# Optimization experiments

Measured on AMD Instinct MI355X. Metric: run time of the kernel, lower is better.

Reference implementation:

```python
import jax, jax.numpy as jnp
import numpy as np

Q_SIZE = 1024
K_SIZE = 1024
NUM_UNITS = 1024
B, T_Q, T_K = 16, 64, 128


def setup_inputs() -> dict:
    key = jax.random.key(0)
    k1, k2, k3, k4, k5 = jax.random.split(key, 5)
    stdv = 1.0 / np.sqrt(NUM_UNITS)
    query = jax.random.normal(k1, (B, T_Q, Q_SIZE), dtype=jnp.float32)
    keys = jax.random.normal(k2, (B, T_K, K_SIZE), dtype=jnp.float32)
    # nn.Linear(in, out, bias=False) weight has shape (out, in)
    Wq = jax.random.uniform(k3, (NUM_UNITS, Q_SIZE), dtype=jnp.float32,
                            minval=-stdv, maxval=stdv)
    Wk = jax.random.uniform(k4, (NUM_UNITS, K_SIZE), dtype=jnp.float32,
                            minval=-stdv, maxval=stdv)
    linear_att = jax.random.uniform(k5, (NUM_UNITS,), dtype=jnp.float32,
                                    minval=-stdv, maxval=stdv)
    normalize_scalar = jnp.full((1,), stdv, dtype=jnp.float32)
    normalize_bias = jnp.zeros((NUM_UNITS,), dtype=jnp.float32)
    return {"query": query, "keys": keys, "Wq": Wq, "Wk": Wk,
            "linear_att": linear_att, "normalize_scalar": normalize_scalar,
            "normalize_bias": normalize_bias}


def reference(query, keys, Wq, Wk, linear_att, normalize_scalar, normalize_bias):
    # batch_first=True, 3-d query, math='fp32', normalize=True, dropout=0, no mask
    att_query = jnp.einsum('bqi,ni->bqn', query, Wq)   # (b, t_q, n)
    att_keys = jnp.einsum('bki,ni->bkn', keys, Wk)     # (b, t_k, n)
    # broadcast sum + bias: (b, t_q, t_k, n)
    sum_qk = att_query[:, :, None, :] + att_keys[:, None, :, :] + normalize_bias
    la = linear_att / jnp.linalg.norm(linear_att)
    la = la * normalize_scalar  # (n,) via broadcast with (1,)
    scores = jnp.einsum('bqkn,n->bqk', jnp.tanh(sum_qk), la)  # (b, t_q, t_k)
    scores_normalized = jax.nn.softmax(scores, axis=-1)
    context = jnp.einsum('bqk,bkn->bqn', scores_normalized, keys)
    return context, scores_normalized
```

## Files before the change

### kernel.cpp

```cpp
#include <hip/hip_runtime.h>
#include <hip/hip_bf16.h>
#include <math.h>


#define ALPHA_2LOG2E 2.8853900817779268f
#define LOG2E 1.4426950408889634f

typedef __attribute__((ext_vector_type(8))) short short8;
typedef __attribute__((ext_vector_type(4))) float f32x4;
typedef __attribute__((ext_vector_type(2))) float f32x2;

static __device__ __forceinline__ short f2bf(float f) {
    union { float f; unsigned u; } v; v.f = f;
    unsigned r = v.u + 0x7fffu + ((v.u >> 16) & 1u);
    return (short)(r >> 16);
}

static __device__ __forceinline__ void gload16(const void* g, void* l) {
    __builtin_amdgcn_global_load_lds(
        (const __attribute__((address_space(1))) unsigned*)g,
        (__attribute__((address_space(3))) unsigned*)l, 16, 0, 0);
}

__global__ __launch_bounds__(256) void cast_prep_kernel(
    const float* __restrict__ q, const float* __restrict__ k,
    const float* __restrict__ wq, const float* __restrict__ wk,
    short* __restrict__ qb, short* __restrict__ kb,
    short* __restrict__ wqb, short* __restrict__ wkb,
    const float* __restrict__ la, const float* __restrict__ scal,
    float* __restrict__ la2, float* __restrict__ sla)
{
    const int bid = blockIdx.x;
    if (bid == 2560) {
        __shared__ float red[4];
        const int t = threadIdx.x, lane = t & 63, w = t >> 6;
        float ss = 0.f;
        for (int i = t; i < 1024; i += 256) { float v = la[i]; ss = fmaf(v, v, ss); }
        #pragma unroll
        for (int off = 32; off; off >>= 1) ss += __shfl_xor(ss, off, 64);
        if (lane == 0) red[w] = ss;
        __syncthreads();
        const float tot = red[0] + red[1] + red[2] + red[3];
        const float sc = scal[0] / sqrtf(tot);
        float s2 = 0.f;
        for (int i = t; i < 1024; i += 256) {
            float v = la[i] * sc;
            la2[i] = 2.f * v;
            s2 += v;
        }
        #pragma unroll
        for (int off = 32; off; off >>= 1) s2 += __shfl_xor(s2, off, 64);
        __syncthreads();
        if (lane == 0) red[w] = s2;
        __syncthreads();
        if (t == 0) sla[0] = red[0] + red[1] + red[2] + red[3];
        return;
    }
    const float* src; short* dst; int base;
    if (bid < 512)       { src = q;  dst = qb;  base = bid; }
    else if (bid < 1536) { src = k;  dst = kb;  base = bid - 512; }
    else if (bid < 2048) { src = wq; dst = wqb; base = bid - 1536; }
    else                 { src = wk; dst = wkb; base = bid - 2048; }
    const size_t i = ((size_t)base * 256 + threadIdx.x) * 8;
    float4 a = *reinterpret_cast<const float4*>(src + i);
    float4 b = *reinterpret_cast<const float4*>(src + i + 4);
    short8 o;
    o[0] = f2bf(a.x); o[1] = f2bf(a.y); o[2] = f2bf(a.z); o[3] = f2bf(a.w);
    o[4] = f2bf(b.x); o[5] = f2bf(b.y); o[6] = f2bf(b.z); o[7] = f2bf(b.w);
    *reinterpret_cast<short8*>(dst + i) = o;
}

__global__ __launch_bounds__(256) void gemm_mfma_kernel(
    const short* __restrict__ qb, const short* __restrict__ kb,
    const short* __restrict__ wqb, const short* __restrict__ wkb,
    const float* __restrict__ bias,
    float* __restrict__ aqE, float* __restrict__ akE)
{
    __shared__ short As[2][64][32];
    __shared__ short Bs[2][64][32];

    const int bid = blockIdx.x;
    const short* A; const short* W; float* C; int useBias, bm, bn, ldc;
    if (bid < 256) {
        A = qb;  W = wqb; C = aqE; useBias = 0; ldc = 1024;
        bm = (bid & 15) * 64; bn = (bid >> 4) * 64;
    } else {
        int b2 = bid - 256;
        A = wkb; W = kb;  C = akE; useBias = 1; ldc = 2048;
        bm = (b2 & 15) * 64; bn = (b2 >> 4) * 64;
    }

    const int t = threadIdx.x;
    const int lane = t & 63, wid = t >> 6;
    const int wr = wid >> 1, wc = wid & 1;
    const int fr = lane & 15, fg = lane >> 4;

    const short* gA0 = A + (size_t)(bm + (wid << 4) + (lane >> 2)) * 1024 + ((lane & 3) << 3);
    const short* gB0 = W + (size_t)(bn + (wid << 4) + (lane >> 2)) * 1024 + ((lane & 3) << 3);

    const f32x4 zero = {0.f, 0.f, 0.f, 0.f};
    f32x4 acc[2][2];
    acc[0][0] = zero; acc[0][1] = zero; acc[1][0] = zero; acc[1][1] = zero;

    gload16(gA0, &As[0][wid << 4][0]);
    gload16(gB0, &Bs[0][wid << 4][0]);
    asm volatile("s_waitcnt vmcnt(0)" ::: "memory");
    __builtin_amdgcn_s_barrier();
    asm volatile("" ::: "memory");

    #pragma unroll 1
    for (int kt = 0; kt < 32; ++kt) {
        const int cur = kt & 1;
        if (kt < 31) {
            const int ko = (kt + 1) << 5;
            gload16(gA0 + ko, &As[cur ^ 1][wid << 4][0]);
            gload16(gB0 + ko, &Bs[cur ^ 1][wid << 4][0]);
        }
        short8 af[2], bfr[2];
        #pragma unroll
        for (int mi = 0; mi < 2; ++mi)
            af[mi] = *(const short8*)&As[cur][wr * 32 + mi * 16 + fr][fg * 8];
        #pragma unroll
        for (int ni = 0; ni < 2; ++ni)
            bfr[ni] = *(const short8*)&Bs[cur][wc * 32 + ni * 16 + fr][fg * 8];
        #pragma unroll
        for (int mi = 0; mi < 2; ++mi)
            #pragma unroll
            for (int ni = 0; ni < 2; ++ni)
                acc[mi][ni] = __builtin_amdgcn_mfma_f32_16x16x32_bf16(
                    af[mi], bfr[ni], acc[mi][ni], 0, 0, 0);
        asm volatile("s_waitcnt vmcnt(0) lgkmcnt(0)" ::: "memory");
        __builtin_amdgcn_s_barrier();
        asm volatile("" ::: "memory");
    }

    float* Cb = C + (size_t)bm * ldc;
    #pragma unroll
    for (int mi = 0; mi < 2; ++mi) {
        const int row0 = wr * 32 + mi * 16 + fg * 4;
        float brow[4] = {0.f, 0.f, 0.f, 0.f};
        if (useBias) {
            #pragma unroll
            for (int r = 0; r < 4; ++r) brow[r] = bias[bm + row0 + r];
        }
        #pragma unroll
        for (int ni = 0; ni < 2; ++ni) {
            const int col = bn + wc * 32 + ni * 16 + fr;
            #pragma unroll
            for (int r = 0; r < 4; ++r)
                Cb[(size_t)(row0 + r) * ldc + col] =
                    __builtin_amdgcn_exp2f((acc[mi][ni][r] + brow[r]) * ALPHA_2LOG2E);
        }
    }
}

__global__ __launch_bounds__(1024) void scores_part_kernel(
    const float* __restrict__ aqE, const float* __restrict__ akE,
    const float* __restrict__ la2, float* __restrict__ partials)
{
    const int b = blockIdx.x, nc = blockIdx.y;
    const int t = threadIdx.x, w = t >> 6, lane = t & 63;

    __shared__ f32x2 eqP[32][64];
    __shared__ float eks[64][128];
    __shared__ float l2s[64];

    {
        const int qq = t >> 4, nj = (t & 15) << 2;
        float4 v = *(const float4*)(aqE + ((size_t)((b << 6) + qq) << 10) + (nc << 6) + nj);
        f32x2 p0 = {v.x, v.y}, p1 = {v.z, v.w};
        eqP[nj >> 1][qq] = p0;
        eqP[(nj >> 1) + 1][qq] = p1;
        const int n = t >> 4, k0 = (t & 15) << 3;
        const float* src = akE + ((size_t)((nc << 6) + n) << 11) + (b << 7) + k0;
        *(float4*)&eks[n][k0]     = *(const float4*)src;
        *(float4*)&eks[n][k0 + 4] = *(const float4*)(src + 4);
        if (t < 64) l2s[t] = la2[(nc << 6) + t];
    }
    __syncthreads();

    const int k0 = w << 3;
    f32x2 acc[4];
    #pragma unroll
    for (int j = 0; j < 4; ++j) acc[j] = (f32x2){0.f, 0.f};

    #pragma unroll 4
    for (int np = 0; np < 32; ++np) {
        const int n0 = np << 1;
        const f32x4 e0a = *(const f32x4*)&eks[n0][k0];
        const f32x4 e0b = *(const f32x4*)&eks[n0][k0 + 4];
        const f32x4 e1a = *(const f32x4*)&eks[n0 + 1][k0];
        const f32x4 e1b = *(const f32x4*)&eks[n0 + 1][k0 + 4];
        const f32x2 l2 = *(const f32x2*)&l2s[n0];
        const float S = l2.x + l2.y;
        const f32x2 eq = eqP[np][lane];
        const f32x2 Svec = {S, S};

        f32x2 ek0[4], ek1[4];
        ek0[0] = (f32x2){e0a.x, e0a.y}; ek0[1] = (f32x2){e0a.z, e0a.w};
        ek0[2] = (f32x2){e0b.x, e0b.y}; ek0[3] = (f32x2){e0b.z, e0b.w};
        ek1[0] = (f32x2){e1a.x, e1a.y}; ek1[1] = (f32x2){e1a.z, e1a.w};
        ek1[2] = (f32x2){e1b.x, e1b.y}; ek1[3] = (f32x2){e1b.z, e1b.w};

        #pragma unroll
        for (int j = 0; j < 4; ++j) {
            const f32x2 E0 = eq.x * ek0[j];
            const f32x2 E1 = eq.y * ek1[j];
            const f32x2 d1 = E1 + 1.f;
            const f32x2 D  = E0 * d1 + d1;
            const f32x2 num = l2.x * E1 + (l2.y * E0 + Svec);
            f32x2 r;
            r.x = __builtin_amdgcn_rcpf(D.x);
            r.y = __builtin_amdgcn_rcpf(D.y);
            acc[j] = num * r + acc[j];
        }
    }

    float* pp = partials + ((size_t)((b << 4) + nc) << 13) + (lane << 7) + k0;
    #pragma unroll
    for (int j = 0; j < 4; ++j)
        *(f32x2*)(pp + (j << 1)) = acc[j];
}

__global__ __launch_bounds__(256) void reduce_softmax_kernel(
    const float* __restrict__ partials, const float* __restrict__ sla,
    float* __restrict__ p_buf, float* __restrict__ out_scores)
{
    const int b = blockIdx.x, qo = blockIdx.y;
    const int t = threadIdx.x, w = t >> 6, lane = t & 63;
    const int q = (qo << 2) + w;

    const float* pp = partials + ((size_t)b << 17) + (q << 7) + (lane << 1);
    float s0 = 0.f, s1 = 0.f;
    #pragma unroll
    for (int nc = 0; nc < 16; ++nc) {
        const float2 v = *(const float2*)(pp + ((size_t)nc << 13));
        s0 += v.x; s1 += v.y;
    }
    const float Sla = sla[0];
    s0 = Sla - s0; s1 = Sla - s1;
    float m = fmaxf(s0, s1);
    #pragma unroll
    for (int off = 32; off; off >>= 1) m = fmaxf(m, __shfl_xor(m, off, 64));
    float e0 = __builtin_amdgcn_exp2f((s0 - m) * LOG2E);
    float e1 = __builtin_amdgcn_exp2f((s1 - m) * LOG2E);
    float s = e0 + e1;
    #pragma unroll
    for (int off = 32; off; off >>= 1) s += __shfl_xor(s, off, 64);
    const float inv = __builtin_amdgcn_rcpf(s);
    float2 p = {e0 * inv, e1 * inv};
    *(float2*)(p_buf + ((size_t)((b << 6) + q) << 7) + (lane << 1)) = p;
    *(float2*)(out_scores + ((size_t)((b << 6) + q) << 7) + (lane << 1)) = p;
}

__global__ __launch_bounds__(512) void ctx_kernel(
    const float* __restrict__ p_buf, const float* __restrict__ keys,
    float* __restrict__ ctx)
{
    const int b = blockIdx.x, nc = blockIdx.y;
    const int t = threadIdx.x;

    __shared__ float ks[128][64];
    __shared__ float ps[64][128];

    {
        const int k = t >> 2, n0 = (t & 3) << 4;
        const float* src = keys + ((size_t)((b << 7) + k) << 10) + (nc << 6) + n0;
        #pragma unroll
        for (int i = 0; i < 4; ++i)
            *(float4*)&ks[k][n0 + (i << 2)] = *(const float4*)(src + (i << 2));
        const int qq = t >> 3, k0 = (t & 7) << 4;
        const float* psrc = p_buf + ((size_t)((b << 6) + qq) << 7) + k0;
        #pragma unroll
        for (int i = 0; i < 4; ++i)
            *(float4*)&ps[qq][k0 + (i << 2)] = *(const float4*)(psrc + (i << 2));
    }
    __syncthreads();

    const int q0 = (t >> 5) << 2;
    const int n0 = (t & 31) << 1;
    float acc[4][2];
    #pragma unroll
    for (int i = 0; i < 4; ++i) { acc[i][0] = 0.f; acc[i][1] = 0.f; }

    #pragma unroll 8
    for (int k = 0; k < 128; ++k) {
        const float2 kv = *(const float2*)&ks[k][n0];
        #pragma unroll
        for (int i = 0; i < 4; ++i) {
            const float p = ps[q0 + i][k];
            acc[i][0] = fmaf(p, kv.x, acc[i][0]);
            acc[i][1] = fmaf(p, kv.y, acc[i][1]);
        }
    }
    #pragma unroll
    for (int i = 0; i < 4; ++i) {
        float2 v = {acc[i][0], acc[i][1]};
        *(float2*)(ctx + ((size_t)((b << 6) + q0 + i) << 10) + (nc << 6) + n0) = v;
    }
}

extern "C" void kernel_launch(void* const* d_in, const int* in_sizes, int n_in,
                              void* d_out, int out_size, void* d_ws, size_t ws_size,
                              hipStream_t stream) {
    const float* query  = (const float*)d_in[0];
    const float* keys   = (const float*)d_in[1];
    const float* Wq     = (const float*)d_in[2];
    const float* Wk     = (const float*)d_in[3];
    const float* la     = (const float*)d_in[4];
    const float* scal   = (const float*)d_in[5];
    const float* bias   = (const float*)d_in[6];

    float* ws  = (float*)d_ws;
    float* aqE = ws;
    float* akE = ws + (1u << 20);
    float* la2 = akE + (2u << 20);
    float* sla = la2 + 1024;
    short* qb  = (short*)(ws + 3 * 1048576 + 2048);
    short* kb  = qb + 1048576;
    short* wqb = kb + 2097152;
    short* wkb = wqb + 1048576;
    float* partials = (float*)kb;
    float* p_buf    = (float*)qb;

    float* ctx        = (float*)d_out;
    float* out_scores = ctx + (size_t)16 * 64 * 1024;

    cast_prep_kernel<<<2561, 256, 0, stream>>>(query, keys, Wq, Wk, qb, kb, wqb, wkb,
                                               la, scal, la2, sla);
    gemm_mfma_kernel<<<768, 256, 0, stream>>>(qb, kb, wqb, wkb, bias, aqE, akE);
    scores_part_kernel<<<dim3(16, 16), 1024, 0, stream>>>(aqE, akE, la2, partials);
    reduce_softmax_kernel<<<dim3(16, 16), 256, 0, stream>>>(partials, sla, p_buf, out_scores);
    ctx_kernel<<<dim3(16, 16), 512, 0, stream>>>(p_buf, keys, ctx);
}
```

Measured before the change: 60.45 us.

## Fuse bf16 cast into GEMM loads and merge softmax with context kernel

```diff
diff --git a/kernel.cpp b/kernel.cpp
--- a/kernel.cpp
+++ b/kernel.cpp
@@ -16,22 +16,23 @@
     return (short)(r >> 16);
 }
 
-static __device__ __forceinline__ void gload16(const void* g, void* l) {
-    __builtin_amdgcn_global_load_lds(
-        (const __attribute__((address_space(1))) unsigned*)g,
-        (__attribute__((address_space(3))) unsigned*)l, 16, 0, 0);
-}
-
-__global__ __launch_bounds__(256) void cast_prep_kernel(
-    const float* __restrict__ q, const float* __restrict__ k,
+static __device__ __forceinline__ short8 cvt8(float4 a, float4 b) {
+    short8 o;
+    o[0] = f2bf(a.x); o[1] = f2bf(a.y); o[2] = f2bf(a.z); o[3] = f2bf(a.w);
+    o[4] = f2bf(b.x); o[5] = f2bf(b.y); o[6] = f2bf(b.z); o[7] = f2bf(b.w);
+    return o;
+}
+
+__global__ __launch_bounds__(256) void gemm_prep_kernel(
+    const float* __restrict__ query, const float* __restrict__ keys,
     const float* __restrict__ wq, const float* __restrict__ wk,
-    short* __restrict__ qb, short* __restrict__ kb,
-    short* __restrict__ wqb, short* __restrict__ wkb,
+    const float* __restrict__ bias,
     const float* __restrict__ la, const float* __restrict__ scal,
+    float* __restrict__ aqE, float* __restrict__ akE,
     float* __restrict__ la2, float* __restrict__ sla)
 {
     const int bid = blockIdx.x;
-    if (bid == 2560) {
+    if (bid == 768) {
         __shared__ float red[4];
         const int t = threadIdx.x, lane = t & 63, w = t >> 6;
         float ss = 0.f;
@@ -56,37 +57,17 @@
         if (t == 0) sla[0] = red[0] + red[1] + red[2] + red[3];
         return;
     }
-    const float* src; short* dst; int base;
-    if (bid < 512)       { src = q;  dst = qb;  base = bid; }
-    else if (bid < 1536) { src = k;  dst = kb;  base = bid - 512; }
-    else if (bid < 2048) { src = wq; dst = wqb; base = bid - 1536; }
-    else                 { src = wk; dst = wkb; base = bid - 2048; }
-    const size_t i = ((size_t)base * 256 + threadIdx.x) * 8;
-    float4 a = *reinterpret_cast<const float4*>(src + i);
-    float4 b = *reinterpret_cast<const float4*>(src + i + 4);
-    short8 o;
-    o[0] = f2bf(a.x); o[1] = f2bf(a.y); o[2] = f2bf(a.z); o[3] = f2bf(a.w);
-    o[4] = f2bf(b.x); o[5] = f2bf(b.y); o[6] = f2bf(b.z); o[7] = f2bf(b.w);
-    *reinterpret_cast<short8*>(dst + i) = o;
-}
-
-__global__ __launch_bounds__(256) void gemm_mfma_kernel(
-    const short* __restrict__ qb, const short* __restrict__ kb,
-    const short* __restrict__ wqb, const short* __restrict__ wkb,
-    const float* __restrict__ bias,
-    float* __restrict__ aqE, float* __restrict__ akE)
-{
+
     __shared__ short As[2][64][32];
     __shared__ short Bs[2][64][32];
 
-    const int bid = blockIdx.x;
-    const short* A; const short* W; float* C; int useBias, bm, bn, ldc;
+    const float* A; const float* W; float* C; int useBias, bm, bn, ldc;
     if (bid < 256) {
-        A = qb;  W = wqb; C = aqE; useBias = 0; ldc = 1024;
+        A = query; W = wq; C = aqE; useBias = 0; ldc = 1024;
         bm = (bid & 15) * 64; bn = (bid >> 4) * 64;
     } else {
         int b2 = bid - 256;
-        A = wkb; W = kb;  C = akE; useBias = 1; ldc = 2048;
+        A = wk; W = keys; C = akE; useBias = 1; ldc = 2048;
         bm = (b2 & 15) * 64; bn = (b2 >> 4) * 64;
     }
 
@@ -95,27 +76,27 @@
     const int wr = wid >> 1, wc = wid & 1;
     const int fr = lane & 15, fg = lane >> 4;
 
-    const short* gA0 = A + (size_t)(bm + (wid << 4) + (lane >> 2)) * 1024 + ((lane & 3) << 3);
-    const short* gB0 = W + (size_t)(bn + (wid << 4) + (lane >> 2)) * 1024 + ((lane & 3) << 3);
+    const int sRow = t >> 2, sSlot = t & 3;
+    const float* gA = A + (size_t)(bm + sRow) * 1024 + (sSlot << 3);
+    const float* gW = W + (size_t)(bn + sRow) * 1024 + (sSlot << 3);
 
     const f32x4 zero = {0.f, 0.f, 0.f, 0.f};
     f32x4 acc[2][2];
     acc[0][0] = zero; acc[0][1] = zero; acc[1][0] = zero; acc[1][1] = zero;
 
-    gload16(gA0, &As[0][wid << 4][0]);
-    gload16(gB0, &Bs[0][wid << 4][0]);
-    asm volatile("s_waitcnt vmcnt(0)" ::: "memory");
+    float4 a0 = *(const float4*)gA,        a1 = *(const float4*)(gA + 4);
+    float4 w0 = *(const float4*)gW,        w1 = *(const float4*)(gW + 4);
+    *(short8*)&As[0][sRow][sSlot << 3] = cvt8(a0, a1);
+    *(short8*)&Bs[0][sRow][sSlot << 3] = cvt8(w0, w1);
+    a0 = *(const float4*)(gA + 32); a1 = *(const float4*)(gA + 36);
+    w0 = *(const float4*)(gW + 32); w1 = *(const float4*)(gW + 36);
+    asm volatile("s_waitcnt lgkmcnt(0)" ::: "memory");
     __builtin_amdgcn_s_barrier();
     asm volatile("" ::: "memory");
 
     #pragma unroll 1
     for (int kt = 0; kt < 32; ++kt) {
         const int cur = kt & 1;
-        if (kt < 31) {
-            const int ko = (kt + 1) << 5;
-            gload16(gA0 + ko, &As[cur ^ 1][wid << 4][0]);
-            gload16(gB0 + ko, &Bs[cur ^ 1][wid << 4][0]);
-        }
         short8 af[2], bfr[2];
         #pragma unroll
         for (int mi = 0; mi < 2; ++mi)
@@ -123,13 +104,22 @@
         #pragma unroll
         for (int ni = 0; ni < 2; ++ni)
             bfr[ni] = *(const short8*)&Bs[cur][wc * 32 + ni * 16 + fr][fg * 8];
+        if (kt < 31) {
+            *(short8*)&As[cur ^ 1][sRow][sSlot << 3] = cvt8(a0, a1);
+            *(short8*)&Bs[cur ^ 1][sRow][sSlot << 3] = cvt8(w0, w1);
+        }
+        if (kt < 30) {
+            const int ko = (kt + 2) << 5;
+            a0 = *(const float4*)(gA + ko);      a1 = *(const float4*)(gA + ko + 4);
+            w0 = *(const float4*)(gW + ko);      w1 = *(const float4*)(gW + ko + 4);
+        }
         #pragma unroll
         for (int mi = 0; mi < 2; ++mi)
             #pragma unroll
             for (int ni = 0; ni < 2; ++ni)
                 acc[mi][ni] = __builtin_amdgcn_mfma_f32_16x16x32_bf16(
                     af[mi], bfr[ni], acc[mi][ni], 0, 0, 0);
-        asm volatile("s_waitcnt vmcnt(0) lgkmcnt(0)" ::: "memory");
+        asm volatile("s_waitcnt lgkmcnt(0)" ::: "memory");
         __builtin_amdgcn_s_barrier();
         asm volatile("" ::: "memory");
     }
@@ -222,46 +212,16 @@
         *(f32x2*)(pp + (j << 1)) = acc[j];
 }
 
-__global__ __launch_bounds__(256) void reduce_softmax_kernel(
+__global__ __launch_bounds__(512) void softmax_ctx_kernel(
     const float* __restrict__ partials, const float* __restrict__ sla,
-    float* __restrict__ p_buf, float* __restrict__ out_scores)
-{
-    const int b = blockIdx.x, qo = blockIdx.y;
-    const int t = threadIdx.x, w = t >> 6, lane = t & 63;
-    const int q = (qo << 2) + w;
-
-    const float* pp = partials + ((size_t)b << 17) + (q << 7) + (lane << 1);
-    float s0 = 0.f, s1 = 0.f;
-    #pragma unroll
-    for (int nc = 0; nc < 16; ++nc) {
-        const float2 v = *(const float2*)(pp + ((size_t)nc << 13));
-        s0 += v.x; s1 += v.y;
-    }
-    const float Sla = sla[0];
-    s0 = Sla - s0; s1 = Sla - s1;
-    float m = fmaxf(s0, s1);
-    #pragma unroll
-    for (int off = 32; off; off >>= 1) m = fmaxf(m, __shfl_xor(m, off, 64));
-    float e0 = __builtin_amdgcn_exp2f((s0 - m) * LOG2E);
-    float e1 = __builtin_amdgcn_exp2f((s1 - m) * LOG2E);
-    float s = e0 + e1;
-    #pragma unroll
-    for (int off = 32; off; off >>= 1) s += __shfl_xor(s, off, 64);
-    const float inv = __builtin_amdgcn_rcpf(s);
-    float2 p = {e0 * inv, e1 * inv};
-    *(float2*)(p_buf + ((size_t)((b << 6) + q) << 7) + (lane << 1)) = p;
-    *(float2*)(out_scores + ((size_t)((b << 6) + q) << 7) + (lane << 1)) = p;
-}
-
-__global__ __launch_bounds__(512) void ctx_kernel(
-    const float* __restrict__ p_buf, const float* __restrict__ keys,
-    float* __restrict__ ctx)
+    const float* __restrict__ keys,
+    float* __restrict__ ctx, float* __restrict__ out_scores)
 {
     const int b = blockIdx.x, nc = blockIdx.y;
-    const int t = threadIdx.x;
-
+    const int t = threadIdx.x, w = t >> 6, lane = t & 63;
+
+    __shared__ float ps[64][128];
     __shared__ float ks[128][64];
-    __shared__ float ps[64][128];
 
     {
         const int k = t >> 2, n0 = (t & 3) << 4;
@@ -269,11 +229,39 @@
         #pragma unroll
         for (int i = 0; i < 4; ++i)
             *(float4*)&ks[k][n0 + (i << 2)] = *(const float4*)(src + (i << 2));
-        const int qq = t >> 3, k0 = (t & 7) << 4;
-        const float* psrc = p_buf + ((size_t)((b << 6) + qq) << 7) + k0;
-        #pragma unroll
-        for (int i = 0; i < 4; ++i)
-            *(float4*)&ps[qq][k0 + (i << 2)] = *(const float4*)(psrc + (i << 2));
+    }
+    #pragma unroll
+    for (int i = 0; i < 8; ++i) {
+        const int e = (i << 9) + t;
+        const int q = e >> 6, kp = e & 63;
+        const float* pq = partials + ((size_t)b << 17) + (q << 7) + (kp << 1);
+        f32x2 s = {0.f, 0.f};
+        #pragma unroll
+        for (int c = 0; c < 16; ++c)
+            s += *(const f32x2*)(pq + ((size_t)c << 13));
+        *(f32x2*)&ps[q][kp << 1] = s;
+    }
+    __syncthreads();
+
+    const float Sla = sla[0];
+    #pragma unroll
+    for (int r = 0; r < 8; ++r) {
+        const int q = (w << 3) + r;
+        const float2 v = *(const float2*)&ps[q][lane << 1];
+        float s0 = Sla - v.x, s1 = Sla - v.y;
+        float m = fmaxf(s0, s1);
+        #pragma unroll
+        for (int off = 32; off; off >>= 1) m = fmaxf(m, __shfl_xor(m, off, 64));
+        float e0 = __builtin_amdgcn_exp2f((s0 - m) * LOG2E);
+        float e1 = __builtin_amdgcn_exp2f((s1 - m) * LOG2E);
+        float s = e0 + e1;
+        #pragma unroll
+        for (int off = 32; off; off >>= 1) s += __shfl_xor(s, off, 64);
+        const float inv = __builtin_amdgcn_rcpf(s);
+        float2 p = {e0 * inv, e1 * inv};
+        *(float2*)&ps[q][lane << 1] = p;
+        if (nc == 0)
+            *(float2*)(out_scores + ((size_t)((b << 6) + q) << 7) + (lane << 1)) = p;
     }
     __syncthreads();
 
@@ -316,20 +304,14 @@
     float* akE = ws + (1u << 20);
     float* la2 = akE + (2u << 20);
     float* sla = la2 + 1024;
-    short* qb  = (short*)(ws + 3 * 1048576 + 2048);
-    short* kb  = qb + 1048576;
-    short* wqb = kb + 2097152;
-    short* wkb = wqb + 1048576;
-    float* partials = (float*)kb;
-    float* p_buf    = (float*)qb;
+    float* partials = sla + 1024;
 
     float* ctx        = (float*)d_out;
     float* out_scores = ctx + (size_t)16 * 64 * 1024;
 
-    cast_prep_kernel<<<2561, 256, 0, stream>>>(query, keys, Wq, Wk, qb, kb, wqb, wkb,
-                                               la, scal, la2, sla);
-    gemm_mfma_kernel<<<768, 256, 0, stream>>>(qb, kb, wqb, wkb, bias, aqE, akE);
+    gemm_prep_kernel<<<769, 256, 0, stream>>>(query, keys, Wq, Wk, bias, la, scal,
+                                              aqE, akE, la2, sla);
     scores_part_kernel<<<dim3(16, 16), 1024, 0, stream>>>(aqE, akE, la2, partials);
-    reduce_softmax_kernel<<<dim3(16, 16), 256, 0, stream>>>(partials, sla, p_buf, out_scores);
-    ctx_kernel<<<dim3(16, 16), 512, 0, stream>>>(p_buf, keys, ctx);
-}
+    softmax_ctx_kernel<<<dim3(16, 16), 512, 0, stream>>>(partials, sla, keys,
+                                                         ctx, out_scores);
+}
```

New measurement: 63.12 us. 1.04x slower.
